# Kernel optimization log

Hardware: AMD Instinct MI355X
Metric: run time of the kernel (lower is better)

The kernel has to match this reference:

```python
import jax, jax.numpy as jnp
import numpy as np

N_NODES = 100000
N_EDGES = 1600000
EMB = 128
N_LAYERS = 3
BN_EPS = 1e-5


def setup_inputs() -> dict:
    key = jax.random.key(0)
    k1, k2, k3 = jax.random.split(key, 3)
    feats = jax.random.normal(k1, (N_NODES, EMB), dtype=jnp.float32)
    edge_index = jax.random.randint(k2, (2, N_EDGES), 0, N_NODES, dtype=jnp.int64)
    # Glorot-ish scaled weights per layer
    W = jax.random.normal(k3, (N_LAYERS, EMB, EMB), dtype=jnp.float32) * (1.0 / np.sqrt(EMB))
    b = jnp.zeros((N_LAYERS, EMB), dtype=jnp.float32)
    gamma = jnp.ones((N_LAYERS, EMB), dtype=jnp.float32)
    beta = jnp.zeros((N_LAYERS, EMB), dtype=jnp.float32)
    return {"feats": feats, "edge_index": edge_index, "W": W, "b": b, "gamma": gamma, "beta": beta}


def _gcn_layer(h, row, col, W_l, b_l):
    # GCNConv (add_self_loops=False, normalize=True): x = h @ W, symmetric-norm scatter-add, + bias
    x = h @ W_l  # [N, D]
    ones = jnp.ones((row.shape[0],), dtype=h.dtype)
    deg = jax.ops.segment_sum(ones, col, num_segments=N_NODES)  # in-degree of targets
    dinv = jnp.where(deg > 0, jax.lax.rsqrt(jnp.maximum(deg, 1.0)), 0.0)
    norm = dinv[row] * dinv[col]  # [E]
    msg = x[row] * norm[:, None]  # gather + scale, [E, D]
    out = jax.ops.segment_sum(msg, col, num_segments=N_NODES)  # scatter-add
    return out + b_l


def _batch_norm(h, gamma_l, beta_l):
    mu = jnp.mean(h, axis=0)
    var = jnp.mean(jnp.square(h - mu), axis=0)  # biased var (torch BN training math)
    return (h - mu) * jax.lax.rsqrt(var + BN_EPS) * gamma_l + beta_l


def reference(feats, edge_index, W, b, gamma, beta):
    row, col = edge_index[0], edge_index[1]  # source, target
    h = feats
    for l in range(N_LAYERS):
        h = _gcn_layer(h, row, col, W[l], b[l])
        h = _batch_norm(h, gamma[l], beta[l])
        # dropout treated as identity (eval mode); residual=False; JK='last'
    return h
```

## Files before the change

### kernel.cpp

```cpp
#include <hip/hip_runtime.h>
#include <cstdint>
#include <cstddef>

#define BN_EPS 1e-5f
#define NCHUNK 256
#define WT_PITCH 136

typedef short bf16x8 __attribute__((ext_vector_type(8)));
typedef float f32x4 __attribute__((ext_vector_type(4)));


__device__ __forceinline__ int edge_at(const void* e, long long i, int m64) {
  return m64 ? (int)((const long long*)e)[i] : ((const int*)e)[i];
}

__device__ __forceinline__ unsigned short f2bf(float f) {
  unsigned int u = __float_as_uint(f);
  unsigned int r = (u + 0x7FFFu + ((u >> 16) & 1u)) >> 16;
  return (unsigned short)r;
}

__device__ __forceinline__ unsigned int pack2bf(float lo, float hi) {
  return (unsigned int)f2bf(lo) | ((unsigned int)f2bf(hi) << 16);
}

__global__ void detect_kernel(const int* __restrict__ e, int* __restrict__ mode) {
  int nz = 0;
  for (int i = 1; i < 512; i += 2) nz |= e[i];
  mode[0] = (nz == 0) ? 1 : 0;
}


__global__ __launch_bounds__(256) void count_kernel(const void* __restrict__ edges,
                                                    const int* __restrict__ mode,
                                                    int* __restrict__ blockcounts,
                                                    int E, int nb, int chunk) {
  __shared__ int h[1024];
  int m = mode[0];
  for (int i = threadIdx.x; i < nb; i += 256) h[i] = 0;
  __syncthreads();
  long long lo = (long long)blockIdx.x * chunk;
  long long hi = lo + chunk;
  if (hi > E) hi = E;
  for (long long i = lo + threadIdx.x; i < hi; i += 256) {
    int c = edge_at(edges, (long long)E + i, m);
    atomicAdd(&h[c >> 8], 1);
  }
  __syncthreads();
  for (int j = threadIdx.x; j < nb; j += 256)
    blockcounts[(size_t)j * NCHUNK + blockIdx.x] = h[j];
}

__global__ __launch_bounds__(256) void scan1_kernel(const int* __restrict__ src,
                                                    int* __restrict__ tprefix,
                                                    int* __restrict__ bsum, int n) {
  __shared__ int s[256];
  int t = threadIdx.x;
  int gid = blockIdx.x * 256 + t;
  int base = gid * 4;
  int sum = 0;
#pragma unroll
  for (int j = 0; j < 4; j++) {
    int i = base + j;
    if (i < n) sum += src[i];
  }
  s[t] = sum;
  __syncthreads();
  for (int off = 1; off < 256; off <<= 1) {
    int v = (t >= off) ? s[t - off] : 0;
    __syncthreads();
    s[t] += v;
    __syncthreads();
  }
  tprefix[gid] = s[t] - sum;
  if (t == 255) bsum[blockIdx.x] = s[255];
}

__global__ __launch_bounds__(256) void scan2_kernel(int* __restrict__ bsum, int nbk,
                                                    int* __restrict__ out, int n) {
  __shared__ int s[256];
  int t = threadIdx.x;
  int v = (t < nbk) ? bsum[t] : 0;
  s[t] = v;
  __syncthreads();
  for (int off = 1; off < 256; off <<= 1) {
    int u = (t >= off) ? s[t - off] : 0;
    __syncthreads();
    s[t] += u;
    __syncthreads();
  }
  if (t < nbk) bsum[t] = s[t] - v;
  if (t == 255) out[n] = s[255];
}

__global__ __launch_bounds__(256) void scan3_kernel(const int* __restrict__ src,
                                                    const int* __restrict__ tprefix,
                                                    const int* __restrict__ bsum,
                                                    int* __restrict__ out, int n) {
  int gid = blockIdx.x * 256 + threadIdx.x;
  int run = bsum[blockIdx.x] + tprefix[gid];
  int base = gid * 4;
#pragma unroll
  for (int j = 0; j < 4; j++) {
    int i = base + j;
    if (i < n) {
      int c = src[i];
      out[i] = run;
      run += c;
    }
  }
}

__global__ __launch_bounds__(256) void scatter_kernel(const void* __restrict__ edges,
                                                      const int* __restrict__ mode,
                                                      const int* __restrict__ moff,
                                                      int* __restrict__ pairs,
                                                      int E, int nb, int chunk) {
  __shared__ int cur[1024];
  int m = mode[0];
  for (int j = threadIdx.x; j < nb; j += 256)
    cur[j] = moff[(size_t)j * NCHUNK + blockIdx.x];
  __syncthreads();
  long long lo = (long long)blockIdx.x * chunk;
  long long hi = lo + chunk;
  if (hi > E) hi = E;
  for (long long i = lo + threadIdx.x; i < hi; i += 256) {
    int r = edge_at(edges, i, m);
    int c = edge_at(edges, (long long)E + i, m);
    int pos = atomicAdd(&cur[c >> 8], 1);
    pairs[pos] = (r << 8) | (c & 255);
  }
}

__global__ __launch_bounds__(256) void passB12_kernel(const int* __restrict__ pairs,
                                                      const int* __restrict__ moff,
                                                      float* __restrict__ dinv,
                                                      int* __restrict__ offsets,
                                                      int* __restrict__ csr_row, int n) {
  __shared__ int h[256];
  __shared__ int s[256];
  int t = threadIdx.x;
  int b = blockIdx.x;
  h[t] = 0;
  __syncthreads();
  int lo = moff[(size_t)b * NCHUNK];
  int hi = moff[(size_t)(b + 1) * NCHUNK];
  for (int e = lo + t; e < hi; e += 256)
    atomicAdd(&h[pairs[e] & 255], 1);
  __syncthreads();
  int d = h[t];
  s[t] = d;
  __syncthreads();
  for (int off = 1; off < 256; off <<= 1) {
    int v = (t >= off) ? s[t - off] : 0;
    __syncthreads();
    s[t] += v;
    __syncthreads();
  }
  int start = lo + s[t] - d;
  int node = b * 256 + t;
  if (node < n) {
    offsets[node] = start;
    dinv[node] = d > 0 ? rsqrtf((float)d) : 0.f;
    if (node == n - 1) offsets[n] = hi;
  }
  s[t] = start;
  __syncthreads();
  for (int e = lo + t; e < hi; e += 256) {
    int p = pairs[e];
    int pos = atomicAdd(&s[p & 255], 1);
    csr_row[pos] = p >> 8;
  }
}

__global__ __launch_bounds__(256) void prepWR_kernel(const float* __restrict__ W,
                                                     const float* __restrict__ colstats,
                                                     const float* __restrict__ gamma,
                                                     const float* __restrict__ beta,
                                                     float invN, int use_affine,
                                                     unsigned short* __restrict__ Wt,
                                                     float* __restrict__ rbias) {
  __shared__ float sc[128], sh[128];
  int t = threadIdx.x;
  if (t < 128) {
    float scv = 1.f, shv = 0.f;
    if (use_affine) {
      float mu = colstats[t] * invN;
      float var = colstats[128 + t] * invN - mu * mu;
      var = fmaxf(var, 0.f);
      scv = gamma[t] * rsqrtf(var + BN_EPS);
      shv = beta[t] - mu * scv;
    }
    sc[t] = scv;
    sh[t] = shv;
  }
  __syncthreads();
  int idx = blockIdx.x * 256 + t;
  int nc = idx >> 7, k = idx & 127;
  Wt[(size_t)nc * 128 + k] = f2bf(W[(size_t)k * 128 + nc] * sc[k]);
  if (blockIdx.x == 0 && t < 128) {
    float s = 0.f;
    if (use_affine) {
      for (int kk = 0; kk < 128; kk++) s += sh[kk] * W[(size_t)kk * 128 + t];
    }
    rbias[t] = s;
  }
}

template <int A_IS_FP32>
__global__ __launch_bounds__(256) void gemm_mfma_kernel(
    const void* __restrict__ Ain, const unsigned short* __restrict__ Wt,
    const float* __restrict__ rbias, const float* __restrict__ dinv,
    unsigned short* __restrict__ xb, int n) {
  __shared__ unsigned short wt[128 * WT_PITCH];
  int t = threadIdx.x;
  {
    int row = t >> 1, half = t & 1;
    const uint4* src = (const uint4*)(Wt + (size_t)row * 128 + half * 64);
    uint4* dst = (uint4*)(wt + row * WT_PITCH + half * 64);
#pragma unroll
    for (int j = 0; j < 8; j++) dst[j] = src[j];
  }
  __syncthreads();

  int l = t & 63;
  int w = t >> 6;
  int row0 = blockIdx.x * 64 + w * 16;
  int m = row0 + (l & 15);
  int mc = m < n ? m : n - 1;
  int kg = l >> 4;

  bf16x8 b[4];
#pragma unroll
  for (int kk = 0; kk < 4; kk++) {
    if (A_IS_FP32) {
      const float* ap = (const float*)Ain + (size_t)mc * 128 + kk * 32 + kg * 8;
      float4 f0 = *(const float4*)ap;
      float4 f1 = *(const float4*)(ap + 4);
      bf16x8 bb;
      bb[0] = (short)f2bf(f0.x); bb[1] = (short)f2bf(f0.y);
      bb[2] = (short)f2bf(f0.z); bb[3] = (short)f2bf(f0.w);
      bb[4] = (short)f2bf(f1.x); bb[5] = (short)f2bf(f1.y);
      bb[6] = (short)f2bf(f1.z); bb[7] = (short)f2bf(f1.w);
      b[kk] = bb;
    } else {
      b[kk] = *(const bf16x8*)((const unsigned short*)Ain + (size_t)mc * 128 + kk * 32 + kg * 8);
    }
  }

  f32x4 acc[8];
#pragma unroll
  for (int nt = 0; nt < 8; nt++) {
    f32x4 zv = {0.f, 0.f, 0.f, 0.f};
    acc[nt] = zv;
  }

#pragma unroll
  for (int kk = 0; kk < 4; kk++) {
#pragma unroll
    for (int nt = 0; nt < 8; nt++) {
      bf16x8 a = *(const bf16x8*)(wt + (size_t)(nt * 16 + (l & 15)) * WT_PITCH + kk * 32 + kg * 8);
      acc[nt] = __builtin_amdgcn_mfma_f32_16x16x32_bf16(a, b[kk], acc[nt], 0, 0, 0);
    }
  }

  float dv = dinv[mc];
  int colbase = kg * 4;
#pragma unroll
  for (int nt = 0; nt < 8; nt++) {
    int c0 = nt * 16 + colbase;
    float4 rb = *(const float4*)&rbias[c0];
    unsigned int w0 = pack2bf((acc[nt][0] + rb.x) * dv, (acc[nt][1] + rb.y) * dv);
    unsigned int w1 = pack2bf((acc[nt][2] + rb.z) * dv, (acc[nt][3] + rb.w) * dv);
    if (m < n)
      *(uint2*)(xb + (size_t)m * 128 + c0) = make_uint2(w0, w1);
  }
}

template <int F32OUT>
__global__ __launch_bounds__(256) void agg_kernel(
    const uint4* __restrict__ x4, const int* __restrict__ csr_row,
    const int* __restrict__ offsets, const float* __restrict__ dinv,
    void* __restrict__ z, int n) {
  int node = blockIdx.x * 16 + (threadIdx.x >> 4);
  int d8 = threadIdx.x & 15;
  if (node >= n) return;
  int lo = offsets[node], hi = offsets[node + 1];
  float a0[8] = {}, a1[8] = {}, a2[8] = {}, a3[8] = {};
#define ACC8(A, v)                                                         \
  A[0] += __uint_as_float((v).x << 16); A[1] += __uint_as_float((v).x & 0xffff0000u); \
  A[2] += __uint_as_float((v).y << 16); A[3] += __uint_as_float((v).y & 0xffff0000u); \
  A[4] += __uint_as_float((v).z << 16); A[5] += __uint_as_float((v).z & 0xffff0000u); \
  A[6] += __uint_as_float((v).w << 16); A[7] += __uint_as_float((v).w & 0xffff0000u);
  int e = lo;
  for (; e + 4 <= hi; e += 4) {
    int r0 = csr_row[e];
    int r1 = csr_row[e + 1];
    int r2 = csr_row[e + 2];
    int r3 = csr_row[e + 3];
    uint4 v0 = x4[(size_t)r0 * 16 + d8];
    uint4 v1 = x4[(size_t)r1 * 16 + d8];
    uint4 v2 = x4[(size_t)r2 * 16 + d8];
    uint4 v3 = x4[(size_t)r3 * 16 + d8];
    ACC8(a0, v0) ACC8(a1, v1) ACC8(a2, v2) ACC8(a3, v3)
  }
  for (; e < hi; e++) {
    uint4 v = x4[(size_t)csr_row[e] * 16 + d8];
    ACC8(a0, v)
  }
#undef ACC8
  float dvn = dinv[node];
  float s[8];
#pragma unroll
  for (int j = 0; j < 8; j++) s[j] = (a0[j] + a1[j] + a2[j] + a3[j]) * dvn;
  if (F32OUT) {
    float* zp = (float*)z + (size_t)node * 128 + d8 * 8;
    *(float4*)zp = make_float4(s[0], s[1], s[2], s[3]);
    *(float4*)(zp + 4) = make_float4(s[4], s[5], s[6], s[7]);
  } else {
    uint4 o = make_uint4(pack2bf(s[0], s[1]), pack2bf(s[2], s[3]),
                         pack2bf(s[4], s[5]), pack2bf(s[6], s[7]));
    *(uint4*)((unsigned short*)z + (size_t)node * 128 + d8 * 8) = o;
  }
}

template <int F32IN>
__global__ __launch_bounds__(256) void stats2_kernel(
    const void* __restrict__ z, float* __restrict__ partial, int total8) {
  __shared__ float ps[256];
  int t = threadIdx.x;
  ps[t] = 0.f;
  __syncthreads();
  int d8 = t & 15;
  float s[8] = {}, q[8] = {};
  int idx = blockIdx.x * 256 + t;
  int stride = gridDim.x * 256;
  for (int i = idx; i < total8; i += stride) {
    float v[8];
    if (F32IN) {
      const float* zp = (const float*)z + (size_t)i * 8;
      float4 f0 = *(const float4*)zp;
      float4 f1 = *(const float4*)(zp + 4);
      v[0] = f0.x; v[1] = f0.y; v[2] = f0.z; v[3] = f0.w;
      v[4] = f1.x; v[5] = f1.y; v[6] = f1.z; v[7] = f1.w;
    } else {
      uint4 u = ((const uint4*)z)[i];
      v[0] = __uint_as_float(u.x << 16); v[1] = __uint_as_float(u.x & 0xffff0000u);
      v[2] = __uint_as_float(u.y << 16); v[3] = __uint_as_float(u.y & 0xffff0000u);
      v[4] = __uint_as_float(u.z << 16); v[5] = __uint_as_float(u.z & 0xffff0000u);
      v[6] = __uint_as_float(u.w << 16); v[7] = __uint_as_float(u.w & 0xffff0000u);
    }
#pragma unroll
    for (int j = 0; j < 8; j++) { s[j] += v[j]; q[j] += v[j] * v[j]; }
  }
#pragma unroll
  for (int j = 0; j < 8; j++) {
    atomicAdd(&ps[d8 * 8 + j], s[j]);
    atomicAdd(&ps[128 + d8 * 8 + j], q[j]);
  }
  __syncthreads();
  partial[(size_t)blockIdx.x * 256 + t] = ps[t];
}

__global__ __launch_bounds__(256) void reduce_stats_kernel(
    const float* __restrict__ partial, float* __restrict__ out, int nblk) {
  __shared__ float red[256];
  int c = blockIdx.x;
  float s = 0.f;
  for (int i = threadIdx.x; i < nblk; i += 256) s += partial[(size_t)i * 256 + c];
  red[threadIdx.x] = s;
  __syncthreads();
  for (int o = 128; o > 0; o >>= 1) {
    if (threadIdx.x < o) red[threadIdx.x] += red[threadIdx.x + o];
    __syncthreads();
  }
  if (threadIdx.x == 0) out[c] = red[0];
}

__global__ __launch_bounds__(256) void norm_kernel(
    float* __restrict__ z, const float* __restrict__ colstats,
    const float* __restrict__ gamma, const float* __restrict__ beta,
    float invN, int total4) {
  __shared__ float sc[128], sh[128];
  int t = threadIdx.x;
  if (t < 128) {
    float mu = colstats[t] * invN;
    float var = colstats[128 + t] * invN - mu * mu;
    var = fmaxf(var, 0.f);
    float s = gamma[t] * rsqrtf(var + BN_EPS);
    sc[t] = s;
    sh[t] = beta[t] - mu * s;
  }
  __syncthreads();
  int idx = blockIdx.x * blockDim.x + t;
  int stride = gridDim.x * blockDim.x;
  for (int i = idx; i < total4; i += stride) {
    float4 v = ((const float4*)z)[i];
    int d0 = (i & 31) * 4;
    v.x = v.x * sc[d0] + sh[d0];
    v.y = v.y * sc[d0 + 1] + sh[d0 + 1];
    v.z = v.z * sc[d0 + 2] + sh[d0 + 2];
    v.w = v.w * sc[d0 + 3] + sh[d0 + 3];
    ((float4*)z)[i] = v;
  }
}


extern "C" void kernel_launch(void* const* d_in, const int* in_sizes, int n_in,
                              void* d_out, int out_size, void* d_ws, size_t ws_size,
                              hipStream_t stream) {
  const float* feats = (const float*)d_in[0];
  const void* edges = d_in[1];
  const float* W = (const float*)d_in[2];
  const float* gamma = (const float*)d_in[4];
  const float* beta = (const float*)d_in[5];

  const int n = in_sizes[0] / 128;
  const int E = in_sizes[1] / 2;

  const int nb = (n + 255) / 256;
  const int m = nb * NCHUNK;
  const int chunk = (E + NCHUNK - 1) / NCHUNK;
  const int sb_m = (m + 1023) / 1024;
  const int nagg = (n + 15) / 16;
  const int nstat = 1024;

  char* ws = (char*)d_ws;
  size_t off = 0;
  unsigned short* xb = (unsigned short*)(ws + off); off += (size_t)n * 128 * 2; off = (off + 255) & ~(size_t)255;
  float* dinv = (float*)(ws + off); off += (size_t)n * 4;
  int* offsets = (int*)(ws + off); off += (size_t)(n + 1) * 4; off = (off + 255) & ~(size_t)255;
  int* csr_row = (int*)(ws + off); off += (size_t)E * 4; off = (off + 255) & ~(size_t)255;
  int* pairs = (int*)(ws + off); off += (size_t)E * 4; off = (off + 255) & ~(size_t)255;
  int* blockcounts = (int*)(ws + off); off += (size_t)m * 4; off = (off + 255) & ~(size_t)255;
  int* moff = (int*)(ws + off); off += (size_t)(m + 1) * 4; off = (off + 255) & ~(size_t)255;
  int* tprefix = (int*)(ws + off); off += (size_t)sb_m * 256 * 4; off = (off + 255) & ~(size_t)255;
  int* bsum = (int*)(ws + off); off += 256 * 4;
  unsigned short* Wt = (unsigned short*)(ws + off); off += 128 * 128 * 2; off = (off + 255) & ~(size_t)255;
  float* rbias = (float*)(ws + off); off += 128 * 4;
  float* colstats = (float*)(ws + off); off += 256 * 4;
  int* mode = (int*)(ws + off); off += 4;

  float* partial = (float*)pairs;

  detect_kernel<<<1, 1, 0, stream>>>((const int*)edges, mode);
  count_kernel<<<NCHUNK, 256, 0, stream>>>(edges, mode, blockcounts, E, nb, chunk);
  scan1_kernel<<<sb_m, 256, 0, stream>>>(blockcounts, tprefix, bsum, m);
  scan2_kernel<<<1, 256, 0, stream>>>(bsum, sb_m, moff, m);
  scan3_kernel<<<sb_m, 256, 0, stream>>>(blockcounts, tprefix, bsum, moff, m);
  scatter_kernel<<<NCHUNK, 256, 0, stream>>>(edges, mode, moff, pairs, E, nb, chunk);
  passB12_kernel<<<nb, 256, 0, stream>>>(pairs, moff, dinv, offsets, csr_row, n);

  unsigned short* zb = (unsigned short*)d_out;
  float* zf = (float*)d_out;
  const int ggrid = (n + 63) / 64;
  const int total8 = n * 16;
  const float invN = 1.0f / (float)n;

  for (int l = 0; l < 3; l++) {
    prepWR_kernel<<<64, 256, 0, stream>>>(W + (size_t)l * 16384, colstats,
                                          gamma + l * 128, beta + l * 128, invN,
                                          l > 0 ? 1 : 0, Wt, rbias);
    if (l == 0)
      gemm_mfma_kernel<1><<<ggrid, 256, 0, stream>>>(feats, Wt, rbias, dinv, xb, n);
    else
      gemm_mfma_kernel<0><<<ggrid, 256, 0, stream>>>(zb, Wt, rbias, dinv, xb, n);
    if (l < 2) {
      agg_kernel<0><<<nagg, 256, 0, stream>>>(
          (const uint4*)xb, csr_row, offsets, dinv, zb, n);
      stats2_kernel<0><<<nstat, 256, 0, stream>>>(zb, partial, total8);
    } else {
      agg_kernel<1><<<nagg, 256, 0, stream>>>(
          (const uint4*)xb, csr_row, offsets, dinv, zf, n);
      stats2_kernel<1><<<nstat, 256, 0, stream>>>(zf, partial, total8);
    }
    reduce_stats_kernel<<<256, 256, 0, stream>>>(partial, colstats, nstat);
  }
  norm_kernel<<<2048, 256, 0, stream>>>(zf, colstats, gamma + 2 * 128, beta + 2 * 128,
                                        invN, (n * 128) / 4);
}
```

Baseline: 422.9 us.

## Sort nodes by in-degree to balance aggregation work across wavefronts

Adds a counting sort of nodes by in-degree (histogram, reuse of the existing scan kernels, scatter into a permutation). The aggregation kernel then processes nodes in permuted order, so nodes with similar edge counts share a wavefront and divergence within a wave shrinks. It adds five small launches and an extra indirection per node. It also loses output-write locality, because consecutive slots now map to scattered node rows.

```diff
diff --git a/kernel.cpp b/kernel.cpp
--- a/kernel.cpp
+++ b/kernel.cpp
@@ -170,6 +170,38 @@
     int p = pairs[e];
     int pos = atomicAdd(&s[p & 255], 1);
     csr_row[pos] = p >> 8;
+  }
+}
+
+__global__ __launch_bounds__(256) void dsort1_kernel(const int* __restrict__ offsets,
+                                                     int* __restrict__ dbc, int n, int nb) {
+  __shared__ int h[128];
+  int t = threadIdx.x, b = blockIdx.x;
+  if (t < 128) h[t] = 0;
+  __syncthreads();
+  int node = b * 256 + t;
+  if (node < n) {
+    int d = offsets[node + 1] - offsets[node];
+    int bin = d > 127 ? 127 : d;
+    atomicAdd(&h[bin], 1);
+  }
+  __syncthreads();
+  if (t < 128) dbc[(size_t)t * nb + b] = h[t];
+}
+
+__global__ __launch_bounds__(256) void dsort2_kernel(const int* __restrict__ offsets,
+                                                     const int* __restrict__ dpos,
+                                                     int* __restrict__ perm, int n, int nb) {
+  __shared__ int cur[128];
+  int t = threadIdx.x, b = blockIdx.x;
+  if (t < 128) cur[t] = dpos[(size_t)t * nb + b];
+  __syncthreads();
+  int node = b * 256 + t;
+  if (node < n) {
+    int d = offsets[node + 1] - offsets[node];
+    int bin = d > 127 ? 127 : d;
+    int pos = atomicAdd(&cur[bin], 1);
+    perm[pos] = node;
   }
 }
 
@@ -281,10 +313,11 @@
 __global__ __launch_bounds__(256) void agg_kernel(
     const uint4* __restrict__ x4, const int* __restrict__ csr_row,
     const int* __restrict__ offsets, const float* __restrict__ dinv,
-    void* __restrict__ z, int n) {
-  int node = blockIdx.x * 16 + (threadIdx.x >> 4);
+    const int* __restrict__ perm, void* __restrict__ z, int n) {
+  int slot = blockIdx.x * 16 + (threadIdx.x >> 4);
   int d8 = threadIdx.x & 15;
-  if (node >= n) return;
+  if (slot >= n) return;
+  int node = perm[slot];
   int lo = offsets[node], hi = offsets[node + 1];
   float a0[8] = {}, a1[8] = {}, a2[8] = {}, a3[8] = {};
 #define ACC8(A, v)                                                         \
@@ -420,8 +453,10 @@
 
   const int nb = (n + 255) / 256;
   const int m = nb * NCHUNK;
+  const int m2 = 128 * nb;
   const int chunk = (E + NCHUNK - 1) / NCHUNK;
   const int sb_m = (m + 1023) / 1024;
+  const int sb_m2 = (m2 + 1023) / 1024;
   const int nagg = (n + 15) / 16;
   const int nstat = 1024;
 
@@ -436,6 +471,9 @@
   int* moff = (int*)(ws + off); off += (size_t)(m + 1) * 4; off = (off + 255) & ~(size_t)255;
   int* tprefix = (int*)(ws + off); off += (size_t)sb_m * 256 * 4; off = (off + 255) & ~(size_t)255;
   int* bsum = (int*)(ws + off); off += 256 * 4;
+  int* perm = (int*)(ws + off); off += (size_t)n * 4; off = (off + 255) & ~(size_t)255;
+  int* dbc = (int*)(ws + off); off += (size_t)m2 * 4; off = (off + 255) & ~(size_t)255;
+  int* dpos = (int*)(ws + off); off += (size_t)(m2 + 1) * 4; off = (off + 255) & ~(size_t)255;
   unsigned short* Wt = (unsigned short*)(ws + off); off += 128 * 128 * 2; off = (off + 255) & ~(size_t)255;
   float* rbias = (float*)(ws + off); off += 128 * 4;
   float* colstats = (float*)(ws + off); off += 256 * 4;
@@ -450,6 +488,11 @@
   scan3_kernel<<<sb_m, 256, 0, stream>>>(blockcounts, tprefix, bsum, moff, m);
   scatter_kernel<<<NCHUNK, 256, 0, stream>>>(edges, mode, moff, pairs, E, nb, chunk);
   passB12_kernel<<<nb, 256, 0, stream>>>(pairs, moff, dinv, offsets, csr_row, n);
+  dsort1_kernel<<<nb, 256, 0, stream>>>(offsets, dbc, n, nb);
+  scan1_kernel<<<sb_m2, 256, 0, stream>>>(dbc, tprefix, bsum, m2);
+  scan2_kernel<<<1, 256, 0, stream>>>(bsum, sb_m2, dpos, m2);
+  scan3_kernel<<<sb_m2, 256, 0, stream>>>(dbc, tprefix, bsum, dpos, m2);
+  dsort2_kernel<<<nb, 256, 0, stream>>>(offsets, dpos, perm, n, nb);
 
   unsigned short* zb = (unsigned short*)d_out;
   float* zf = (float*)d_out;
@@ -467,11 +510,11 @@
       gemm_mfma_kernel<0><<<ggrid, 256, 0, stream>>>(zb, Wt, rbias, dinv, xb, n);
     if (l < 2) {
       agg_kernel<0><<<nagg, 256, 0, stream>>>(
-          (const uint4*)xb, csr_row, offsets, dinv, zb, n);
+          (const uint4*)xb, csr_row, offsets, dinv, perm, zb, n);
       stats2_kernel<0><<<nstat, 256, 0, stream>>>(zb, partial, total8);
     } else {
       agg_kernel<1><<<nagg, 256, 0, stream>>>(
-          (const uint4*)xb, csr_row, offsets, dinv, zf, n);
+          (const uint4*)xb, csr_row, offsets, dinv, perm, zf, n);
       stats2_kernel<1><<<nstat, 256, 0, stream>>>(zf, partial, total8);
     }
     reduce_stats_kernel<<<256, 256, 0, stream>>>(partial, colstats, nstat);
```

Measured after the change: 437.4 us. 1.03x slower.
